# Optimization experiments

Hardware: AMD Instinct MI355X
Metric: run time of the kernel (lower is better)

## Reference

```python
import jax, jax.numpy as jnp
import numpy as np

T, B, H = 2048, 32, 1024

def setup_inputs() -> dict:
    key = jax.random.key(0)
    k1, k2, k3, k4 = jax.random.split(key, 4)
    hidden = jax.random.normal(k1, (1, B, H), dtype=jnp.float32)
    encoderOutput = jax.random.normal(k2, (T, B, H), dtype=jnp.float32)
    # nn.Linear(H, H): weight [H, H], bias [H]
    W = jax.random.normal(k3, (H, H), dtype=jnp.float32) * (1.0 / np.sqrt(H))
    b = jax.random.normal(k4, (H,), dtype=jnp.float32) * 0.01
    return {"hidden": hidden, "encoderOutput": encoderOutput, "W": W, "b": b}

def reference(hidden, encoderOutput, W, b):
    # energy[t,b,:] = W @ encoderOutput[t,b] + bias   (nn.Linear)
    energy = jnp.einsum('tbh,kh->tbk', encoderOutput, W) + b  # [T,B,H]
    # score[b,t] = hidden[0,b] . energy[t,b]
    scores = jnp.einsum('bh,tbh->bt', hidden[0], energy)  # [B,T]
    return jax.nn.softmax(scores, axis=-1)[:, None, :]  # [B,1,T]
```

## Files before the change

kernel.cpp:

```cpp
#include <hip/hip_runtime.h>
#include <math.h>

#define T_DIM 2048
#define B_DIM 32
#define H_DIM 1024

__global__ void __launch_bounds__(256) compute_v_kernel(
    const float* __restrict__ hidden,
    const float* __restrict__ W,
    float* __restrict__ v) {
    const int b = blockIdx.y;
    const int h = blockIdx.x * 256 + threadIdx.x;

    __shared__ float hsh[H_DIM];
    #pragma unroll
    for (int i = 0; i < H_DIM / 256; ++i)
        hsh[i * 256 + threadIdx.x] = hidden[b * H_DIM + i * 256 + threadIdx.x];
    __syncthreads();

    float acc = 0.f;
    #pragma unroll 8
    for (int k = 0; k < H_DIM; ++k)
        acc = fmaf(hsh[k], W[(size_t)k * H_DIM + h], acc);

    v[b * H_DIM + h] = acc;
}

__global__ void __launch_bounds__(256) compute_scores_kernel(
    const float* __restrict__ enc,
    const float* __restrict__ v,
    float* __restrict__ scores) {
    const int b    = blockIdx.y;
    const int wave = threadIdx.x >> 6;
    const int lane = threadIdx.x & 63;
    const int t    = blockIdx.x * 4 + wave;

    __shared__ float vsh[H_DIM];
    {
        const float4* src = (const float4*)(v + b * H_DIM);
        float4*       dst = (float4*)vsh;
        dst[threadIdx.x] = src[threadIdx.x];
    }
    __syncthreads();

    const float4* row = (const float4*)(enc + ((size_t)t * B_DIM + b) * H_DIM);
    const float4* vv4 = (const float4*)vsh;

    float acc = 0.f;
    #pragma unroll
    for (int p = 0; p < H_DIM / (64 * 4); ++p) {
        float4 e = row[p * 64 + lane];
        float4 w = vv4[p * 64 + lane];
        acc = fmaf(e.x, w.x, acc);
        acc = fmaf(e.y, w.y, acc);
        acc = fmaf(e.z, w.z, acc);
        acc = fmaf(e.w, w.w, acc);
    }

    #pragma unroll
    for (int off = 32; off > 0; off >>= 1)
        acc += __shfl_down(acc, off, 64);

    if (lane == 0) scores[b * T_DIM + t] = acc;
}

__global__ void __launch_bounds__(256) softmax_kernel(
    const float* __restrict__ scores,
    float* __restrict__ out) {
    const int b    = blockIdx.x;
    const int tid  = threadIdx.x;
    const int lane = tid & 63;
    const int wv   = tid >> 6;

    const float* row = scores + b * T_DIM;
    float vals[T_DIM / 256];

    float lmax = -INFINITY;
    #pragma unroll
    for (int i = 0; i < T_DIM / 256; ++i) {
        vals[i] = row[i * 256 + tid];
        lmax = fmaxf(lmax, vals[i]);
    }

    __shared__ float redm[4];
    #pragma unroll
    for (int off = 32; off > 0; off >>= 1)
        lmax = fmaxf(lmax, __shfl_xor(lmax, off, 64));
    if (lane == 0) redm[wv] = lmax;
    __syncthreads();
    const float bmax = fmaxf(fmaxf(redm[0], redm[1]), fmaxf(redm[2], redm[3]));

    float lsum = 0.f;
    #pragma unroll
    for (int i = 0; i < T_DIM / 256; ++i) {
        vals[i] = expf(vals[i] - bmax);
        lsum += vals[i];
    }

    __shared__ float reds[4];
    #pragma unroll
    for (int off = 32; off > 0; off >>= 1)
        lsum += __shfl_xor(lsum, off, 64);
    if (lane == 0) reds[wv] = lsum;
    __syncthreads();
    const float inv = 1.0f / (reds[0] + reds[1] + reds[2] + reds[3]);

    #pragma unroll
    for (int i = 0; i < T_DIM / 256; ++i)
        out[b * T_DIM + i * 256 + tid] = vals[i] * inv;
}

extern "C" void kernel_launch(void* const* d_in, const int* in_sizes, int n_in,
                              void* d_out, int out_size, void* d_ws, size_t ws_size,
                              hipStream_t stream) {
    const float* hidden = (const float*)d_in[0];
    const float* enc    = (const float*)d_in[1];
    const float* W      = (const float*)d_in[2];
    float* out = (float*)d_out;

    float* v      = (float*)d_ws;
    float* scores = (float*)((char*)d_ws + (size_t)B_DIM * H_DIM * sizeof(float));

    compute_v_kernel<<<dim3(H_DIM / 256, B_DIM), 256, 0, stream>>>(hidden, W, v);
    compute_scores_kernel<<<dim3(T_DIM / 4, B_DIM), 256, 0, stream>>>(enc, v, scores);
    softmax_kernel<<<B_DIM, 256, 0, stream>>>(scores, out);
}
```

Measured before the change: 432.9 us.

## Split-K the v projection with atomics and compute two rows per wave

```diff
diff --git a/kernel.cpp b/kernel.cpp
--- a/kernel.cpp
+++ b/kernel.cpp
@@ -4,26 +4,25 @@
 #define T_DIM 2048
 #define B_DIM 32
 #define H_DIM 1024
+#define KSPLIT 8
+#define KCHUNK (H_DIM / KSPLIT)
 
 __global__ void __launch_bounds__(256) compute_v_kernel(
     const float* __restrict__ hidden,
     const float* __restrict__ W,
     float* __restrict__ v) {
-    const int b = blockIdx.y;
-    const int h = blockIdx.x * 256 + threadIdx.x;
-
-    __shared__ float hsh[H_DIM];
-    #pragma unroll
-    for (int i = 0; i < H_DIM / 256; ++i)
-        hsh[i * 256 + threadIdx.x] = hidden[b * H_DIM + i * 256 + threadIdx.x];
-    __syncthreads();
+    const int b  = blockIdx.y;
+    const int h  = blockIdx.x * 256 + threadIdx.x;
+    const int k0 = blockIdx.z * KCHUNK;
+    const float* hrow = hidden + b * H_DIM + k0;
+    const float* wcol = W + (size_t)k0 * H_DIM + h;
 
     float acc = 0.f;
-    #pragma unroll 8
-    for (int k = 0; k < H_DIM; ++k)
-        acc = fmaf(hsh[k], W[(size_t)k * H_DIM + h], acc);
+    #pragma unroll 16
+    for (int k = 0; k < KCHUNK; ++k)
+        acc = fmaf(hrow[k], wcol[(size_t)k * H_DIM], acc);
 
-    v[b * H_DIM + h] = acc;
+    atomicAdd(&v[b * H_DIM + h], acc);
 }
 
 __global__ void __launch_bounds__(256) compute_scores_kernel(
@@ -33,35 +32,41 @@
     const int b    = blockIdx.y;
     const int wave = threadIdx.x >> 6;
     const int lane = threadIdx.x & 63;
-    const int t    = blockIdx.x * 4 + wave;
+    const int t0   = blockIdx.x * 8 + wave * 2;
 
     __shared__ float vsh[H_DIM];
     {
         const float4* src = (const float4*)(v + b * H_DIM);
-        float4*       dst = (float4*)vsh;
-        dst[threadIdx.x] = src[threadIdx.x];
+        ((float4*)vsh)[threadIdx.x] = src[threadIdx.x];
     }
     __syncthreads();
 
-    const float4* row = (const float4*)(enc + ((size_t)t * B_DIM + b) * H_DIM);
-    const float4* vv4 = (const float4*)vsh;
+    const float4* row0 = (const float4*)(enc + ((size_t)t0 * B_DIM + b) * H_DIM);
+    const float4* row1 = row0 + (B_DIM * H_DIM) / 4;
+    const float4* vv4  = (const float4*)vsh;
 
-    float acc = 0.f;
+    float acc0 = 0.f, acc1 = 0.f;
     #pragma unroll
     for (int p = 0; p < H_DIM / (64 * 4); ++p) {
-        float4 e = row[p * 64 + lane];
-        float4 w = vv4[p * 64 + lane];
-        acc = fmaf(e.x, w.x, acc);
-        acc = fmaf(e.y, w.y, acc);
-        acc = fmaf(e.z, w.z, acc);
-        acc = fmaf(e.w, w.w, acc);
+        const float4 w  = vv4[p * 64 + lane];
+        const float4 e0 = row0[p * 64 + lane];
+        const float4 e1 = row1[p * 64 + lane];
+        acc0 = fmaf(e0.x, w.x, acc0); acc1 = fmaf(e1.x, w.x, acc1);
+        acc0 = fmaf(e0.y, w.y, acc0); acc1 = fmaf(e1.y, w.y, acc1);
+        acc0 = fmaf(e0.z, w.z, acc0); acc1 = fmaf(e1.z, w.z, acc1);
+        acc0 = fmaf(e0.w, w.w, acc0); acc1 = fmaf(e1.w, w.w, acc1);
     }
 
     #pragma unroll
-    for (int off = 32; off > 0; off >>= 1)
-        acc += __shfl_down(acc, off, 64);
+    for (int off = 32; off > 0; off >>= 1) {
+        acc0 += __shfl_down(acc0, off, 64);
+        acc1 += __shfl_down(acc1, off, 64);
+    }
 
-    if (lane == 0) scores[b * T_DIM + t] = acc;
+    if (lane == 0) {
+        scores[b * T_DIM + t0]     = acc0;
+        scores[b * T_DIM + t0 + 1] = acc1;
+    }
 }
 
 __global__ void __launch_bounds__(256) softmax_kernel(
@@ -121,7 +126,8 @@
     float* v      = (float*)d_ws;
     float* scores = (float*)((char*)d_ws + (size_t)B_DIM * H_DIM * sizeof(float));
 
-    compute_v_kernel<<<dim3(H_DIM / 256, B_DIM), 256, 0, stream>>>(hidden, W, v);
-    compute_scores_kernel<<<dim3(T_DIM / 4, B_DIM), 256, 0, stream>>>(enc, v, scores);
+    hipMemsetAsync(v, 0, (size_t)B_DIM * H_DIM * sizeof(float), stream);
+    compute_v_kernel<<<dim3(H_DIM / 256, B_DIM, KSPLIT), 256, 0, stream>>>(hidden, W, v);
+    compute_scores_kernel<<<dim3(T_DIM / 8, B_DIM), 256, 0, stream>>>(enc, v, scores);
     softmax_kernel<<<B_DIM, 256, 0, stream>>>(scores, out);
 }
```

Measured after the change: 396.1 us. -8.5%, faster.
